# Optimization experiments

Measured on AMD Instinct MI355X. Metric: run time of the kernel, lower is better.

Reference implementation:

```python
import jax, jax.numpy as jnp
import numpy as np

DROPOUT_RATE = 0.5
CONF_THRESH = 0.85
IGNORE_VALUE = 2
EPS = 1e-07


def setup_inputs() -> dict:
    key = jax.random.key(0)
    k1, k2 = jax.random.split(key)
    B, H, W = 16, 1024, 1024
    pred = jax.random.uniform(k1, (B, H, W), dtype=jnp.float32)
    mask = jax.random.randint(k2, (B, H, W), 0, 3, dtype=jnp.int32)
    return {"pred": pred, "mask": mask}


def _training_need_score(pred, gt, confidence):
    # Higher = needs more training: CW=4, UW=3, UC=2, CC=1 (+/- confidence bonus)
    is_correct = (pred > 0.5) == (gt == 1.0)
    is_conf = confidence > CONF_THRESH
    score = jnp.where(is_conf & is_correct, 1.0,
            jnp.where(~is_conf & is_correct, 2.0,
            jnp.where(~is_conf & ~is_correct, 3.0, 4.0))).astype(pred.dtype)
    bonus = (confidence - 0.5) * 0.5
    return jnp.where(is_correct, score - bonus, score + bonus)


def _dynamic_masks(pred, mask):
    # Vectorized equivalent of the per-batch nonzero/argsort/scatter loop:
    # rank annotated pixels per batch by descending need-score; top n_train -> train.
    B, H, W = mask.shape
    annotated = (mask != IGNORE_VALUE).reshape(B, H * W)
    gt = mask.astype(pred.dtype)
    confidence = jnp.maximum(pred, 1.0 - pred)
    scores = _training_need_score(pred, gt, confidence).reshape(B, H * W)
    neg_inf = jnp.asarray(-jnp.inf, scores.dtype)
    masked_scores = jnp.where(annotated, scores, neg_inf)
    order = jnp.argsort(-masked_scores, axis=1)          # descending score order
    rank = jnp.argsort(order, axis=1)                    # rank of each pixel in that order
    n_points = annotated.sum(axis=1)
    n_train = (n_points.astype(jnp.float32) * (1.0 - DROPOUT_RATE)).astype(jnp.int32)
    train = annotated & (rank < n_train[:, None])
    holdout = annotated & ~train
    return train.reshape(B, H, W), holdout.reshape(B, H, W)


def reference(pred, mask):
    if pred.ndim == 4 and pred.shape[1] == 1:
        pred = pred[:, 0]
    train_mask, holdout_mask = _dynamic_masks(pred, mask)
    gt = mask.astype(pred.dtype)
    p = jnp.clip(pred, EPS, 1.0 - EPS)
    bce = -(gt * jnp.log(p) + (1.0 - gt) * jnp.log(1.0 - p))
    tm = train_mask.astype(pred.dtype)
    loss = (bce * tm).sum() / (tm.sum() + EPS)
    return loss, train_mask, holdout_mask
```

## Files before the change

### kernel.cpp

```cpp
#include <hip/hip_runtime.h>
#include <stdint.h>

#define NBATCH 16
#define HW_ (1 << 20)
#define TPB 256

#define NBPB_H 32
#define TPB_H 1024
#define EPB_H (HW_ / NBPB_H)
#define ITER_H (EPB_H / (TPB_H * 4))

#define NBINS 8192
#define FBASE 0x3F400

#define NRED_PB 8
#define WPB ((NBINS / 2) / NRED_PB)

#define NBPB_F 256
#define FCHUNK (HW_ / NBPB_F)

#define CAND_CAP 32768
#define LCAP 512
#define TIE_CAP 4096
#define CNT_STRIDE 64

typedef float f4v __attribute__((ext_vector_type(4)));

struct BParams {
    unsigned int k;
    unsigned int bin1f;
    unsigned int r;
    unsigned int mode;
};

__device__ __forceinline__ unsigned int score_bits(float p, int m) {
    bool correct = (p > 0.5f) == (m == 1);
    float conf = fmaxf(p, 1.0f - p);
    float base = correct ? ((conf > 0.85f) ? 1.0f : 2.0f)
                         : ((conf > 0.85f) ? 4.0f : 3.0f);
    float bonus = (conf - 0.5f) * 0.5f;
    float s = correct ? (base - bonus) : (base + bonus);
    return __float_as_uint(s);
}

__global__ void k_hist1(const float4* __restrict__ pred4, const int4* __restrict__ mask4,
                        unsigned int* __restrict__ hist_part16) {
    __shared__ unsigned int lh[NBINS];
    int b = blockIdx.x / NBPB_H;
    int blk = blockIdx.x % NBPB_H;
    int t = threadIdx.x;
    for (int i = t; i < NBINS; i += TPB_H) lh[i] = 0;
    __syncthreads();
    size_t gb = (size_t)b * (HW_ / 4) + (size_t)blk * (EPB_H / 4);
    float4 p = pred4[gb + t];
    int4 m = mask4[gb + t];
#pragma unroll
    for (int j = 0; j < ITER_H; j++) {
        float4 pc = p;
        int4 mc = m;
        if (j + 1 < ITER_H) {
            p = pred4[gb + (size_t)(j + 1) * TPB_H + t];
            m = mask4[gb + (size_t)(j + 1) * TPB_H + t];
        }
        float pa[4] = {pc.x, pc.y, pc.z, pc.w};
        int ma[4] = {mc.x, mc.y, mc.z, mc.w};
#pragma unroll
        for (int l = 0; l < 4; l++) {
            if (ma[l] != 2) {
                unsigned int sb = score_bits(pa[l], ma[l]);
                int fb = (int)(sb >> 12) - FBASE;
                fb = min(max(fb, 0), NBINS - 1);
                atomicAdd(&lh[fb], 1u);
            }
        }
    }
    __syncthreads();
    unsigned int* hp = hist_part16 + (size_t)(b * NBPB_H + blk) * (NBINS / 2);
    for (int w = t; w < NBINS / 2; w += TPB_H)
        hp[w] = (lh[2 * w] & 0xFFFFu) | (lh[2 * w + 1] << 16);
}

__global__ void k_reduce(const unsigned int* __restrict__ hist_part16,
                         unsigned int* __restrict__ hist1) {
    int b = blockIdx.x / NRED_PB;
    int sb = blockIdx.x % NRED_PB;
    int t = threadIdx.x;
    unsigned int c00 = 0, c01 = 0, c10 = 0, c11 = 0;
#pragma unroll
    for (int p = 0; p < NBPB_H; p++) {
        const unsigned int* hp =
            hist_part16 + (size_t)(b * NBPB_H + p) * (NBINS / 2) + sb * WPB;
        unsigned int w0 = hp[t];
        unsigned int w1 = hp[t + TPB];
        c00 += w0 & 0xFFFFu; c01 += w0 >> 16;
        c10 += w1 & 0xFFFFu; c11 += w1 >> 16;
    }
    uint2* ob = (uint2*)(hist1 + (size_t)b * NBINS + 2 * (size_t)(sb * WPB));
    uint2 o0 = {c00, c01}, o1 = {c10, c11};
    ob[t] = o0;
    ob[t + TPB] = o1;
}

__global__ void k_find1(const unsigned int* __restrict__ hist1, BParams* prm) {
    int b = blockIdx.x;
    int t = threadIdx.x;
    __shared__ unsigned int cs_[257];
    const unsigned int* h = hist1 + (size_t)b * NBINS;
    {
        const uint4* h4 = (const uint4*)(h + t * 32);
        unsigned int s = 0;
#pragma unroll
        for (int j = 0; j < 8; j++) { uint4 v = h4[j]; s += v.x + v.y + v.z + v.w; }
        cs_[t] = s;
        if (t == 0) cs_[256] = 0;
    }
    __syncthreads();
    for (int off = 1; off < 256; off <<= 1) {
        unsigned int a = (t + off < 256) ? cs_[t + off] : 0u;
        __syncthreads();
        cs_[t] += a;
        __syncthreads();
    }
    unsigned int n = cs_[0];
    unsigned int k = (unsigned int)(int)((float)n * 0.5f);
    if (k == 0) {
        if (t == 0) {
            BParams P;
            P.k = 0; P.bin1f = 0xFFFFFFFFu; P.r = 0; P.mode = 0;
            prm[b] = P;
        }
        return;
    }
    if (cs_[t] >= k && cs_[t + 1] < k) {
        unsigned int cum = cs_[t + 1];
        for (int j = 31; j >= 0; j--) {
            unsigned int hb = h[t * 32 + j];
            if (cum + hb >= k) {
                BParams P;
                P.k = k;
                P.bin1f = (unsigned int)(FBASE + t * 32 + j);
                P.r = k - cum;
                P.mode = 1;
                prm[b] = P;
                break;
            }
            cum += hb;
        }
    }
}

__global__ void k_main(const float4* __restrict__ pred4, const int4* __restrict__ mask4,
                       const BParams* __restrict__ prm, float* __restrict__ out,
                       float* __restrict__ partials, unsigned int* __restrict__ cand_cnt,
                       unsigned int* __restrict__ cand_idx, unsigned int* __restrict__ cand_sb,
                       float* __restrict__ cand_bce) {
    int b = blockIdx.x / NBPB_F;
    int blk = blockIdx.x % NBPB_F;
    BParams P = prm[b];
    unsigned int target = P.bin1f;
    __shared__ unsigned int lcode[FCHUNK / 4];
    __shared__ float red[TPB];
    __shared__ unsigned int l_idx[LCAP];
    __shared__ unsigned int l_sb[LCAP];
    __shared__ float l_bce[LCAP];
    __shared__ unsigned int lcnt;
    __shared__ unsigned int gbase;
    if (threadIdx.x == 0) lcnt = 0;
    __syncthreads();
    float acc = 0.0f;
    int ibase = blk * FCHUNK;
    size_t base4 = (size_t)b * (HW_ / 4) + (size_t)(ibase / 4);
    float4 p = pred4[base4 + threadIdx.x];
    int4 m = mask4[base4 + threadIdx.x];
#pragma unroll
    for (int j = 0; j < FCHUNK / (TPB * 4); j++) {
        int v = j * TPB + threadIdx.x;
        float4 pc = p;
        int4 mc = m;
        if (j + 1 < FCHUNK / (TPB * 4)) {
            p = pred4[base4 + (size_t)(j + 1) * TPB + threadIdx.x];
            m = mask4[base4 + (size_t)(j + 1) * TPB + threadIdx.x];
        }
        float pa[4] = {pc.x, pc.y, pc.z, pc.w};
        int ma[4] = {mc.x, mc.y, mc.z, mc.w};
        unsigned int cw = 0;
#pragma unroll
        for (int l = 0; l < 4; l++) {
            bool ann = (ma[l] != 2);
            unsigned int sb = score_bits(pa[l], ma[l]);
            unsigned int fine = sb >> 12;
            bool tr = ann && (fine > target);
            bool amb = ann && (fine == target);
            unsigned int code = (tr ? 1u : 0u) | ((ann && !tr) ? 2u : 0u);
            cw |= code << (8 * l);
            float bce = 0.0f;
            if (tr || amb) {
                float pc2 = fminf(fmaxf(pa[l], 1e-7f), 1.0f - 1e-7f);
                bce = (ma[l] == 1) ? -__logf(pc2) : -__logf(1.0f - pc2);
            }
            if (tr) acc += bce;
            if (amb) {
                unsigned int p0 = atomicAdd(&lcnt, 1u);
                if (p0 < LCAP) {
                    l_idx[p0] = (unsigned int)(ibase + v * 4 + l);
                    l_sb[p0] = sb;
                    l_bce[p0] = bce;
                } else {
                    unsigned int gp = atomicAdd(&cand_cnt[b * CNT_STRIDE], 1u);
                    if (gp < CAND_CAP) {
                        size_t o = (size_t)b * CAND_CAP + gp;
                        cand_idx[o] = (unsigned int)(ibase + v * 4 + l);
                        cand_sb[o] = sb;
                        cand_bce[o] = bce;
                    }
                }
            }
        }
        lcode[v] = cw;
    }
    __syncthreads();
    unsigned int n = min(lcnt, (unsigned int)LCAP);
    if (threadIdx.x == 0 && n > 0)
        gbase = atomicAdd(&cand_cnt[b * CNT_STRIDE], n);
    __syncthreads();
    for (unsigned int i = threadIdx.x; i < n; i += TPB) {
        unsigned int pos = gbase + i;
        if (pos < CAND_CAP) {
            size_t o = (size_t)b * CAND_CAP + pos;
            cand_idx[o] = l_idx[i];
            cand_sb[o] = l_sb[i];
            cand_bce[o] = l_bce[i];
        }
    }
    float* trout = out + 1;
    float* hoout = out + 1 + (size_t)NBATCH * HW_;
    size_t Gbase = (size_t)b * HW_ + (size_t)ibase;
    for (int v = threadIdx.x; v < FCHUNK / 4 - 1; v += TPB) {
        unsigned int w0 = lcode[v];
        unsigned int w1 = lcode[v + 1];
        unsigned int c0 = (w0 >> 24) & 0xFFu;
        unsigned int c1 = w1 & 0xFFu;
        unsigned int c2 = (w1 >> 8) & 0xFFu;
        unsigned int c3 = (w1 >> 16) & 0xFFu;
        int e = 3 + 4 * v;
        f4v tv = { (float)(c0 & 1u), (float)(c1 & 1u), (float)(c2 & 1u), (float)(c3 & 1u) };
        f4v hv = { (float)((c0 >> 1) & 1u), (float)((c1 >> 1) & 1u),
                   (float)((c2 >> 1) & 1u), (float)((c3 >> 1) & 1u) };
        *(f4v*)(trout + Gbase + e) = tv;
        *(f4v*)(hoout + Gbase + e) = hv;
    }
    if (threadIdx.x < 3) {
        unsigned int c = (lcode[0] >> (8 * threadIdx.x)) & 0xFFu;
        trout[Gbase + threadIdx.x] = (float)(c & 1u);
        hoout[Gbase + threadIdx.x] = (float)((c >> 1) & 1u);
    }
    if (threadIdx.x == 3) {
        unsigned int c = (lcode[FCHUNK / 4 - 1] >> 24) & 0xFFu;
        trout[Gbase + FCHUNK - 1] = (float)(c & 1u);
        hoout[Gbase + FCHUNK - 1] = (float)((c >> 1) & 1u);
    }
    red[threadIdx.x] = acc;
    __syncthreads();
    for (int off = TPB / 2; off > 0; off >>= 1) {
        if (threadIdx.x < off) red[threadIdx.x] += red[threadIdx.x + off];
        __syncthreads();
    }
    if (threadIdx.x == 0) partials[blockIdx.x] = red[0];
}

__global__ void k_fixup(const unsigned int* __restrict__ cand_cnt,
                        const unsigned int* __restrict__ cand_idx,
                        const unsigned int* __restrict__ cand_sb,
                        const float* __restrict__ cand_bce,
                        const BParams* __restrict__ prm, float* __restrict__ out,
                        float* __restrict__ tie_partials) {
    int b = blockIdx.x;
    int t = threadIdx.x;
    __shared__ unsigned int h[4096];
    __shared__ unsigned int cs_[257];
    __shared__ unsigned int tie_idx[TIE_CAP];
    __shared__ unsigned int misc[8];
    __shared__ float red[TPB];
    BParams P = prm[b];
    if (P.mode == 0) {
        if (t == 0) tie_partials[b] = 0.0f;
        return;
    }
    unsigned int C = cand_cnt[b * CNT_STRIDE];
    if (C > CAND_CAP) C = CAND_CAP;
    const unsigned int* ci = cand_idx + (size_t)b * CAND_CAP;
    const unsigned int* cs = cand_sb + (size_t)b * CAND_CAP;
    const float* cb = cand_bce + (size_t)b * CAND_CAP;
    for (int i = t; i < 4096; i += TPB) h[i] = 0;
    if (t < 8) misc[t] = (t == 4) ? 0xFFFFFFFFu : 0u;
    __syncthreads();
    for (unsigned int i = t; i < C; i += TPB)
        atomicAdd(&h[cs[i] & 0xFFFu], 1u);
    __syncthreads();
    {
        unsigned int gs = 0;
#pragma unroll
        for (int j = 0; j < 16; j++) gs += h[t * 16 + j];
        cs_[t] = gs;
        if (t == 0) cs_[256] = 0;
    }
    __syncthreads();
    for (int off = 1; off < 256; off <<= 1) {
        unsigned int a = (t + off < 256) ? cs_[t + off] : 0u;
        __syncthreads();
        cs_[t] += a;
        __syncthreads();
    }
    if (cs_[t] >= P.r && cs_[t + 1] < P.r) {
        unsigned int cum = cs_[t + 1];
        for (int j = 15; j >= 0; j--) {
            unsigned int hb = h[t * 16 + j];
            if (cum + hb >= P.r) {
                unsigned int T = P.r - cum;
                misc[0] = (unsigned int)(t * 16 + j);
                misc[1] = T;
                misc[2] = (T == hb) ? 1u : 0u;
                break;
            }
            cum += hb;
        }
    }
    __syncthreads();
    unsigned int vstar = misc[0], T = misc[1];
    bool allTies = (misc[2] != 0);
    unsigned int idxcut;
    if (allTies) {
        idxcut = 0xFFFFFFFFu;
    } else {
        for (unsigned int i = t; i < C; i += TPB) {
            if ((cs[i] & 0xFFFu) == vstar) {
                unsigned int p = atomicAdd(&misc[3], 1u);
                if (p < TIE_CAP) tie_idx[p] = ci[i];
            }
        }
        __syncthreads();
        unsigned int E2 = misc[3];
        if (E2 > TIE_CAP) E2 = TIE_CAP;
        for (unsigned int i = t; i < E2; i += TPB) {
            unsigned int vi = tie_idx[i];
            unsigned int cnt = 0;
            for (unsigned int j = 0; j < E2; j++) cnt += (tie_idx[j] < vi) ? 1u : 0u;
            if (cnt == T - 1) misc[4] = vi;
        }
        __syncthreads();
        idxcut = misc[4];
    }
    float acc = 0.0f;
    float* trout = out + 1;
    float* hoout = out + 1 + (size_t)NBATCH * HW_;
    size_t base = (size_t)b * HW_;
    for (unsigned int i = t; i < C; i += TPB) {
        unsigned int low = cs[i] & 0xFFFu;
        bool tr = (low > vstar) || (low == vstar && ci[i] <= idxcut);
        if (tr) {
            trout[base + ci[i]] = 1.0f;
            hoout[base + ci[i]] = 0.0f;
            acc += cb[i];
        }
    }
    red[t] = acc;
    __syncthreads();
    for (int off = TPB / 2; off > 0; off >>= 1) {
        if (t < off) red[t] += red[t + off];
        __syncthreads();
    }
    if (t == 0) tie_partials[b] = red[0];
}

__global__ void k_loss(const float* __restrict__ partials, const float* __restrict__ tie_partials,
                       const BParams* __restrict__ prm, float* __restrict__ out) {
    __shared__ double red[TPB];
    double s = 0.0;
    for (int i = threadIdx.x; i < NBATCH * NBPB_F; i += TPB) s += (double)partials[i];
    if (threadIdx.x < NBATCH) s += (double)tie_partials[threadIdx.x];
    red[threadIdx.x] = s;
    __syncthreads();
    for (int off = TPB / 2; off > 0; off >>= 1) {
        if (threadIdx.x < off) red[threadIdx.x] += red[threadIdx.x + off];
        __syncthreads();
    }
    if (threadIdx.x == 0) {
        unsigned long long den = 0;
        for (int b = 0; b < NBATCH; b++) den += prm[b].k;
        float denf = (float)den + 1e-7f;
        out[0] = (float)red[0] / denf;
    }
}

extern "C" void kernel_launch(void* const* d_in, const int* in_sizes, int n_in,
                              void* d_out, int out_size, void* d_ws, size_t ws_size,
                              hipStream_t stream) {
    const float4* pred4 = (const float4*)d_in[0];
    const int4* mask4 = (const int4*)d_in[1];
    float* out = (float*)d_out;

    unsigned int* cand_cnt = (unsigned int*)d_ws;
    BParams* prm = (BParams*)(cand_cnt + NBATCH * CNT_STRIDE);
    float* partials = (float*)(prm + NBATCH);
    float* tie_partials = partials + NBATCH * NBPB_F;
    unsigned int* cand_idx = (unsigned int*)(tie_partials + NBATCH);
    unsigned int* cand_sb = cand_idx + NBATCH * CAND_CAP;
    float* cand_bce = (float*)(cand_sb + NBATCH * CAND_CAP);
    unsigned int* hist1 = (unsigned int*)(cand_bce + NBATCH * CAND_CAP);
    unsigned int* hist_part16 = hist1 + NBATCH * NBINS;

    size_t zero_bytes = (size_t)(NBATCH * CNT_STRIDE) * 4;
    hipMemsetAsync(d_ws, 0, zero_bytes, stream);

    k_hist1<<<dim3(NBATCH * NBPB_H), dim3(TPB_H), 0, stream>>>(pred4, mask4, hist_part16);
    k_reduce<<<dim3(NBATCH * NRED_PB), dim3(TPB), 0, stream>>>(hist_part16, hist1);
    k_find1<<<dim3(NBATCH), dim3(TPB), 0, stream>>>(hist1, prm);
    k_main<<<dim3(NBATCH * NBPB_F), dim3(TPB), 0, stream>>>(pred4, mask4, prm, out, partials,
                                                            cand_cnt, cand_idx, cand_sb, cand_bce);
    k_fixup<<<dim3(NBATCH), dim3(TPB), 0, stream>>>(cand_cnt, cand_idx, cand_sb, cand_bce,
                                                    prm, out, tie_partials);
    k_loss<<<dim3(1), dim3(TPB), 0, stream>>>(partials, tie_partials, prm, out);
}
```

Before: 289.4 us.

## Fuse histogram reduce/find and fixup/loss kernels; write masks inline via shuffles

Merges the histogram reduction and threshold-find kernels into a single 1024-thread-per-batch kernel that keeps per-thread bin counts in registers. It also folds the final loss reduction into the fixup kernel, using a last-block-done atomic counter. In the main kernel, mask outputs are written inside the load loop using a wavefront shuffle instead of a separate pass over shared memory, with wave-boundary elements patched afterwards. This removes two kernel launches and a shared-memory pass, but the combined reduce runs on only 16 blocks, which lowers parallelism.

```diff
diff --git a/kernel.cpp b/kernel.cpp
--- a/kernel.cpp
+++ b/kernel.cpp
@@ -13,8 +13,7 @@
 #define NBINS 8192
 #define FBASE 0x3F400
 
-#define NRED_PB 8
-#define WPB ((NBINS / 2) / NRED_PB)
+#define TPB_RF 1024
 
 #define NBPB_F 256
 #define FCHUNK (HW_ / NBPB_F)
@@ -43,6 +42,10 @@
     return __float_as_uint(s);
 }
 
+__device__ __forceinline__ float agent_load_f32(const float* p) {
+    return __hip_atomic_load(p, __ATOMIC_RELAXED, __HIP_MEMORY_SCOPE_AGENT);
+}
+
 __global__ void k_hist1(const float4* __restrict__ pred4, const int4* __restrict__ mask4,
                         unsigned int* __restrict__ hist_part16) {
     __shared__ unsigned int lh[NBINS];
@@ -80,43 +83,31 @@
         hp[w] = (lh[2 * w] & 0xFFFFu) | (lh[2 * w + 1] << 16);
 }
 
-__global__ void k_reduce(const unsigned int* __restrict__ hist_part16,
-                         unsigned int* __restrict__ hist1) {
-    int b = blockIdx.x / NRED_PB;
-    int sb = blockIdx.x % NRED_PB;
-    int t = threadIdx.x;
-    unsigned int c00 = 0, c01 = 0, c10 = 0, c11 = 0;
-#pragma unroll
-    for (int p = 0; p < NBPB_H; p++) {
-        const unsigned int* hp =
-            hist_part16 + (size_t)(b * NBPB_H + p) * (NBINS / 2) + sb * WPB;
-        unsigned int w0 = hp[t];
-        unsigned int w1 = hp[t + TPB];
-        c00 += w0 & 0xFFFFu; c01 += w0 >> 16;
-        c10 += w1 & 0xFFFFu; c11 += w1 >> 16;
-    }
-    uint2* ob = (uint2*)(hist1 + (size_t)b * NBINS + 2 * (size_t)(sb * WPB));
-    uint2 o0 = {c00, c01}, o1 = {c10, c11};
-    ob[t] = o0;
-    ob[t + TPB] = o1;
-}
-
-__global__ void k_find1(const unsigned int* __restrict__ hist1, BParams* prm) {
+__global__ void k_redfind(const unsigned int* __restrict__ hist_part16,
+                          BParams* __restrict__ prm) {
     int b = blockIdx.x;
     int t = threadIdx.x;
-    __shared__ unsigned int cs_[257];
-    const unsigned int* h = hist1 + (size_t)b * NBINS;
-    {
-        const uint4* h4 = (const uint4*)(h + t * 32);
-        unsigned int s = 0;
-#pragma unroll
-        for (int j = 0; j < 8; j++) { uint4 v = h4[j]; s += v.x + v.y + v.z + v.w; }
-        cs_[t] = s;
-        if (t == 0) cs_[256] = 0;
-    }
-    __syncthreads();
-    for (int off = 1; off < 256; off <<= 1) {
-        unsigned int a = (t + off < 256) ? cs_[t + off] : 0u;
+    __shared__ unsigned int cs_[TPB_RF + 1];
+    unsigned int c[8];
+#pragma unroll
+    for (int j = 0; j < 8; j++) c[j] = 0;
+#pragma unroll
+    for (int p = 0; p < NBPB_H; p++) {
+        const uint4* hp = (const uint4*)(hist_part16 + (size_t)(b * NBPB_H + p) * (NBINS / 2));
+        uint4 w = hp[t];
+        c[0] += w.x & 0xFFFFu; c[1] += w.x >> 16;
+        c[2] += w.y & 0xFFFFu; c[3] += w.y >> 16;
+        c[4] += w.z & 0xFFFFu; c[5] += w.z >> 16;
+        c[6] += w.w & 0xFFFFu; c[7] += w.w >> 16;
+    }
+    unsigned int s = 0;
+#pragma unroll
+    for (int j = 0; j < 8; j++) s += c[j];
+    cs_[t] = s;
+    if (t == 0) cs_[TPB_RF] = 0;
+    __syncthreads();
+    for (int off = 1; off < TPB_RF; off <<= 1) {
+        unsigned int a = (t + off < TPB_RF) ? cs_[t + off] : 0u;
         __syncthreads();
         cs_[t] += a;
         __syncthreads();
@@ -133,12 +124,13 @@
     }
     if (cs_[t] >= k && cs_[t + 1] < k) {
         unsigned int cum = cs_[t + 1];
-        for (int j = 31; j >= 0; j--) {
-            unsigned int hb = h[t * 32 + j];
+#pragma unroll
+        for (int j = 7; j >= 0; j--) {
+            unsigned int hb = c[j];
             if (cum + hb >= k) {
                 BParams P;
                 P.k = k;
-                P.bin1f = (unsigned int)(FBASE + t * 32 + j);
+                P.bin1f = (unsigned int)(FBASE + t * 8 + j);
                 P.r = k - cum;
                 P.mode = 1;
                 prm[b] = P;
@@ -170,6 +162,10 @@
     float acc = 0.0f;
     int ibase = blk * FCHUNK;
     size_t base4 = (size_t)b * (HW_ / 4) + (size_t)(ibase / 4);
+    float* trout = out + 1;
+    float* hoout = out + 1 + (size_t)NBATCH * HW_;
+    size_t Gbase = (size_t)b * HW_ + (size_t)ibase;
+    int lane = threadIdx.x & 63;
     float4 p = pred4[base4 + threadIdx.x];
     int4 m = mask4[base4 + threadIdx.x];
 #pragma unroll
@@ -217,6 +213,19 @@
             }
         }
         lcode[v] = cw;
+        unsigned int nw = (unsigned int)__shfl_down((int)cw, 1);
+        if (lane != 63) {
+            unsigned int c0 = cw >> 24;
+            unsigned int c1 = nw & 0xFFu;
+            unsigned int c2 = (nw >> 8) & 0xFFu;
+            unsigned int c3 = (nw >> 16) & 0xFFu;
+            int e = 3 + 4 * v;
+            f4v tv = { (float)(c0 & 1u), (float)(c1 & 1u), (float)(c2 & 1u), (float)(c3 & 1u) };
+            f4v hv = { (float)((c0 >> 1) & 1u), (float)((c1 >> 1) & 1u),
+                       (float)((c2 >> 1) & 1u), (float)((c3 >> 1) & 1u) };
+            *(f4v*)(trout + Gbase + e) = tv;
+            *(f4v*)(hoout + Gbase + e) = hv;
+        }
     }
     __syncthreads();
     unsigned int n = min(lcnt, (unsigned int)LCAP);
@@ -232,29 +241,31 @@
             cand_bce[o] = l_bce[i];
         }
     }
-    float* trout = out + 1;
-    float* hoout = out + 1 + (size_t)NBATCH * HW_;
-    size_t Gbase = (size_t)b * HW_ + (size_t)ibase;
-    for (int v = threadIdx.x; v < FCHUNK / 4 - 1; v += TPB) {
-        unsigned int w0 = lcode[v];
-        unsigned int w1 = lcode[v + 1];
-        unsigned int c0 = (w0 >> 24) & 0xFFu;
-        unsigned int c1 = w1 & 0xFFu;
-        unsigned int c2 = (w1 >> 8) & 0xFFu;
-        unsigned int c3 = (w1 >> 16) & 0xFFu;
-        int e = 3 + 4 * v;
-        f4v tv = { (float)(c0 & 1u), (float)(c1 & 1u), (float)(c2 & 1u), (float)(c3 & 1u) };
-        f4v hv = { (float)((c0 >> 1) & 1u), (float)((c1 >> 1) & 1u),
-                   (float)((c2 >> 1) & 1u), (float)((c3 >> 1) & 1u) };
-        *(f4v*)(trout + Gbase + e) = tv;
-        *(f4v*)(hoout + Gbase + e) = hv;
-    }
-    if (threadIdx.x < 3) {
-        unsigned int c = (lcode[0] >> (8 * threadIdx.x)) & 0xFFu;
-        trout[Gbase + threadIdx.x] = (float)(c & 1u);
-        hoout[Gbase + threadIdx.x] = (float)((c >> 1) & 1u);
-    }
-    if (threadIdx.x == 3) {
+    if (threadIdx.x < 16) {
+        int j = threadIdx.x >> 2, w = threadIdx.x & 3;
+        int v = j * TPB + w * 64 + 63;
+        if (v < FCHUNK / 4 - 1) {
+            unsigned int w0 = lcode[v];
+            unsigned int w1 = lcode[v + 1];
+            unsigned int c0 = w0 >> 24;
+            unsigned int c1 = w1 & 0xFFu;
+            unsigned int c2 = (w1 >> 8) & 0xFFu;
+            unsigned int c3 = (w1 >> 16) & 0xFFu;
+            int e = 3 + 4 * v;
+            f4v tv = { (float)(c0 & 1u), (float)(c1 & 1u), (float)(c2 & 1u), (float)(c3 & 1u) };
+            f4v hv = { (float)((c0 >> 1) & 1u), (float)((c1 >> 1) & 1u),
+                       (float)((c2 >> 1) & 1u), (float)((c3 >> 1) & 1u) };
+            *(f4v*)(trout + Gbase + e) = tv;
+            *(f4v*)(hoout + Gbase + e) = hv;
+        }
+    }
+    if (threadIdx.x >= 16 && threadIdx.x < 19) {
+        int i = threadIdx.x - 16;
+        unsigned int c = (lcode[0] >> (8 * i)) & 0xFFu;
+        trout[Gbase + i] = (float)(c & 1u);
+        hoout[Gbase + i] = (float)((c >> 1) & 1u);
+    }
+    if (threadIdx.x == 19) {
         unsigned int c = (lcode[FCHUNK / 4 - 1] >> 24) & 0xFFu;
         trout[Gbase + FCHUNK - 1] = (float)(c & 1u);
         hoout[Gbase + FCHUNK - 1] = (float)((c >> 1) & 1u);
@@ -273,7 +284,9 @@
                         const unsigned int* __restrict__ cand_sb,
                         const float* __restrict__ cand_bce,
                         const BParams* __restrict__ prm, float* __restrict__ out,
-                        float* __restrict__ tie_partials) {
+                        float* __restrict__ tie_partials,
+                        const float* __restrict__ partials,
+                        unsigned int* __restrict__ done_f) {
     int b = blockIdx.x;
     int t = threadIdx.x;
     __shared__ unsigned int h[4096];
@@ -281,114 +294,118 @@
     __shared__ unsigned int tie_idx[TIE_CAP];
     __shared__ unsigned int misc[8];
     __shared__ float red[TPB];
+    __shared__ double redd[TPB];
+    __shared__ unsigned int lastf;
     BParams P = prm[b];
-    if (P.mode == 0) {
-        if (t == 0) tie_partials[b] = 0.0f;
-        return;
-    }
-    unsigned int C = cand_cnt[b * CNT_STRIDE];
-    if (C > CAND_CAP) C = CAND_CAP;
-    const unsigned int* ci = cand_idx + (size_t)b * CAND_CAP;
-    const unsigned int* cs = cand_sb + (size_t)b * CAND_CAP;
-    const float* cb = cand_bce + (size_t)b * CAND_CAP;
-    for (int i = t; i < 4096; i += TPB) h[i] = 0;
-    if (t < 8) misc[t] = (t == 4) ? 0xFFFFFFFFu : 0u;
-    __syncthreads();
-    for (unsigned int i = t; i < C; i += TPB)
-        atomicAdd(&h[cs[i] & 0xFFFu], 1u);
-    __syncthreads();
-    {
-        unsigned int gs = 0;
-#pragma unroll
-        for (int j = 0; j < 16; j++) gs += h[t * 16 + j];
-        cs_[t] = gs;
-        if (t == 0) cs_[256] = 0;
-    }
-    __syncthreads();
-    for (int off = 1; off < 256; off <<= 1) {
-        unsigned int a = (t + off < 256) ? cs_[t + off] : 0u;
-        __syncthreads();
-        cs_[t] += a;
-        __syncthreads();
-    }
-    if (cs_[t] >= P.r && cs_[t + 1] < P.r) {
-        unsigned int cum = cs_[t + 1];
-        for (int j = 15; j >= 0; j--) {
-            unsigned int hb = h[t * 16 + j];
-            if (cum + hb >= P.r) {
-                unsigned int T = P.r - cum;
-                misc[0] = (unsigned int)(t * 16 + j);
-                misc[1] = T;
-                misc[2] = (T == hb) ? 1u : 0u;
-                break;
-            }
-            cum += hb;
-        }
-    }
-    __syncthreads();
-    unsigned int vstar = misc[0], T = misc[1];
-    bool allTies = (misc[2] != 0);
-    unsigned int idxcut;
-    if (allTies) {
-        idxcut = 0xFFFFFFFFu;
-    } else {
+    float tieval = 0.0f;
+    if (P.mode != 0) {
+        unsigned int C = cand_cnt[b * CNT_STRIDE];
+        if (C > CAND_CAP) C = CAND_CAP;
+        const unsigned int* ci = cand_idx + (size_t)b * CAND_CAP;
+        const unsigned int* cs = cand_sb + (size_t)b * CAND_CAP;
+        const float* cb = cand_bce + (size_t)b * CAND_CAP;
+        for (int i = t; i < 4096; i += TPB) h[i] = 0;
+        if (t < 8) misc[t] = (t == 4) ? 0xFFFFFFFFu : 0u;
+        __syncthreads();
+        for (unsigned int i = t; i < C; i += TPB)
+            atomicAdd(&h[cs[i] & 0xFFFu], 1u);
+        __syncthreads();
+        {
+            unsigned int gs = 0;
+#pragma unroll
+            for (int j = 0; j < 16; j++) gs += h[t * 16 + j];
+            cs_[t] = gs;
+            if (t == 0) cs_[256] = 0;
+        }
+        __syncthreads();
+        for (int off = 1; off < 256; off <<= 1) {
+            unsigned int a = (t + off < 256) ? cs_[t + off] : 0u;
+            __syncthreads();
+            cs_[t] += a;
+            __syncthreads();
+        }
+        if (cs_[t] >= P.r && cs_[t + 1] < P.r) {
+            unsigned int cum = cs_[t + 1];
+            for (int j = 15; j >= 0; j--) {
+                unsigned int hb = h[t * 16 + j];
+                if (cum + hb >= P.r) {
+                    unsigned int T = P.r - cum;
+                    misc[0] = (unsigned int)(t * 16 + j);
+                    misc[1] = T;
+                    misc[2] = (T == hb) ? 1u : 0u;
+                    break;
+                }
+                cum += hb;
+            }
+        }
+        __syncthreads();
+        unsigned int vstar = misc[0], T = misc[1];
+        bool allTies = (misc[2] != 0);
+        unsigned int idxcut;
+        if (allTies) {
+            idxcut = 0xFFFFFFFFu;
+        } else {
+            for (unsigned int i = t; i < C; i += TPB) {
+                if ((cs[i] & 0xFFFu) == vstar) {
+                    unsigned int p = atomicAdd(&misc[3], 1u);
+                    if (p < TIE_CAP) tie_idx[p] = ci[i];
+                }
+            }
+            __syncthreads();
+            unsigned int E2 = misc[3];
+            if (E2 > TIE_CAP) E2 = TIE_CAP;
+            for (unsigned int i = t; i < E2; i += TPB) {
+                unsigned int vi = tie_idx[i];
+                unsigned int cnt = 0;
+                for (unsigned int j = 0; j < E2; j++) cnt += (tie_idx[j] < vi) ? 1u : 0u;
+                if (cnt == T - 1) misc[4] = vi;
+            }
+            __syncthreads();
+            idxcut = misc[4];
+        }
+        float acc = 0.0f;
+        float* trout = out + 1;
+        float* hoout = out + 1 + (size_t)NBATCH * HW_;
+        size_t base = (size_t)b * HW_;
         for (unsigned int i = t; i < C; i += TPB) {
-            if ((cs[i] & 0xFFFu) == vstar) {
-                unsigned int p = atomicAdd(&misc[3], 1u);
-                if (p < TIE_CAP) tie_idx[p] = ci[i];
-            }
-        }
-        __syncthreads();
-        unsigned int E2 = misc[3];
-        if (E2 > TIE_CAP) E2 = TIE_CAP;
-        for (unsigned int i = t; i < E2; i += TPB) {
-            unsigned int vi = tie_idx[i];
-            unsigned int cnt = 0;
-            for (unsigned int j = 0; j < E2; j++) cnt += (tie_idx[j] < vi) ? 1u : 0u;
-            if (cnt == T - 1) misc[4] = vi;
-        }
-        __syncthreads();
-        idxcut = misc[4];
-    }
-    float acc = 0.0f;
-    float* trout = out + 1;
-    float* hoout = out + 1 + (size_t)NBATCH * HW_;
-    size_t base = (size_t)b * HW_;
-    for (unsigned int i = t; i < C; i += TPB) {
-        unsigned int low = cs[i] & 0xFFFu;
-        bool tr = (low > vstar) || (low == vstar && ci[i] <= idxcut);
-        if (tr) {
-            trout[base + ci[i]] = 1.0f;
-            hoout[base + ci[i]] = 0.0f;
-            acc += cb[i];
-        }
-    }
-    red[t] = acc;
+            unsigned int low = cs[i] & 0xFFFu;
+            bool tr = (low > vstar) || (low == vstar && ci[i] <= idxcut);
+            if (tr) {
+                trout[base + ci[i]] = 1.0f;
+                hoout[base + ci[i]] = 0.0f;
+                acc += cb[i];
+            }
+        }
+        red[t] = acc;
+        __syncthreads();
+        for (int off = TPB / 2; off > 0; off >>= 1) {
+            if (t < off) red[t] += red[t + off];
+            __syncthreads();
+        }
+        if (t == 0) tieval = red[0];
+    }
+    if (t == 0)
+        __hip_atomic_store(&tie_partials[b], tieval, __ATOMIC_RELAXED, __HIP_MEMORY_SCOPE_AGENT);
+    __threadfence();
+    __syncthreads();
+    if (t == 0) lastf = (atomicAdd(done_f, 1u) == (unsigned int)(NBATCH - 1)) ? 1u : 0u;
+    __syncthreads();
+    if (!lastf) return;
+    __threadfence();
+    double s = 0.0;
+    for (int i = t; i < NBATCH * NBPB_F; i += TPB) s += (double)partials[i];
+    if (t < NBATCH) s += (double)agent_load_f32(&tie_partials[t]);
+    redd[t] = s;
     __syncthreads();
     for (int off = TPB / 2; off > 0; off >>= 1) {
-        if (t < off) red[t] += red[t + off];
-        __syncthreads();
-    }
-    if (t == 0) tie_partials[b] = red[0];
-}
-
-__global__ void k_loss(const float* __restrict__ partials, const float* __restrict__ tie_partials,
-                       const BParams* __restrict__ prm, float* __restrict__ out) {
-    __shared__ double red[TPB];
-    double s = 0.0;
-    for (int i = threadIdx.x; i < NBATCH * NBPB_F; i += TPB) s += (double)partials[i];
-    if (threadIdx.x < NBATCH) s += (double)tie_partials[threadIdx.x];
-    red[threadIdx.x] = s;
-    __syncthreads();
-    for (int off = TPB / 2; off > 0; off >>= 1) {
-        if (threadIdx.x < off) red[threadIdx.x] += red[threadIdx.x + off];
-        __syncthreads();
-    }
-    if (threadIdx.x == 0) {
+        if (t < off) redd[t] += redd[t + off];
+        __syncthreads();
+    }
+    if (t == 0) {
         unsigned long long den = 0;
-        for (int b = 0; b < NBATCH; b++) den += prm[b].k;
+        for (int b2 = 0; b2 < NBATCH; b2++) den += prm[b2].k;
         float denf = (float)den + 1e-7f;
-        out[0] = (float)red[0] / denf;
+        out[0] = (float)redd[0] / denf;
     }
 }
 
@@ -400,24 +417,22 @@
     float* out = (float*)d_out;
 
     unsigned int* cand_cnt = (unsigned int*)d_ws;
-    BParams* prm = (BParams*)(cand_cnt + NBATCH * CNT_STRIDE);
+    unsigned int* done_f = cand_cnt + NBATCH * CNT_STRIDE;
+    BParams* prm = (BParams*)(done_f + 32);
     float* partials = (float*)(prm + NBATCH);
     float* tie_partials = partials + NBATCH * NBPB_F;
     unsigned int* cand_idx = (unsigned int*)(tie_partials + NBATCH);
     unsigned int* cand_sb = cand_idx + NBATCH * CAND_CAP;
     float* cand_bce = (float*)(cand_sb + NBATCH * CAND_CAP);
-    unsigned int* hist1 = (unsigned int*)(cand_bce + NBATCH * CAND_CAP);
-    unsigned int* hist_part16 = hist1 + NBATCH * NBINS;
-
-    size_t zero_bytes = (size_t)(NBATCH * CNT_STRIDE) * 4;
+    unsigned int* hist_part16 = (unsigned int*)(cand_bce + NBATCH * CAND_CAP);
+
+    size_t zero_bytes = (size_t)(NBATCH * CNT_STRIDE + 32) * 4;
     hipMemsetAsync(d_ws, 0, zero_bytes, stream);
 
     k_hist1<<<dim3(NBATCH * NBPB_H), dim3(TPB_H), 0, stream>>>(pred4, mask4, hist_part16);
-    k_reduce<<<dim3(NBATCH * NRED_PB), dim3(TPB), 0, stream>>>(hist_part16, hist1);
-    k_find1<<<dim3(NBATCH), dim3(TPB), 0, stream>>>(hist1, prm);
+    k_redfind<<<dim3(NBATCH), dim3(TPB_RF), 0, stream>>>(hist_part16, prm);
     k_main<<<dim3(NBATCH * NBPB_F), dim3(TPB), 0, stream>>>(pred4, mask4, prm, out, partials,
                                                             cand_cnt, cand_idx, cand_sb, cand_bce);
     k_fixup<<<dim3(NBATCH), dim3(TPB), 0, stream>>>(cand_cnt, cand_idx, cand_sb, cand_bce,
-                                                    prm, out, tie_partials);
-    k_loss<<<dim3(1), dim3(TPB), 0, stream>>>(partials, tie_partials, prm, out);
-}
+                                                    prm, out, tie_partials, partials, done_f);
+}
```

New measurement: 295.4 us. 2.1% more time.
